# Kernel tuning notes

Measured on AMD Instinct MI355X. Metric: run time of the kernel, lower is better.

## Reference

```python
import jax, jax.numpy as jnp
import numpy as np

B, T, D_MODEL = 2, 2048, 1024
H, D = 16, 64
NEG = -1e9


def setup_inputs() -> dict:
    key = jax.random.key(0)
    k1, k2, k3 = jax.random.split(key, 3)
    x = jax.random.normal(k1, (B, T, D_MODEL), dtype=jnp.float32)
    # causal additive bias: 0 at valid (j<=i), large negative otherwise
    causal = jnp.tril(jnp.ones((T, T), dtype=bool))
    mask = jnp.where(causal, 0.0, NEG).astype(jnp.float32)[None, None]
    # params (torch Linear no-bias; stored as [in, out] so y = x @ W)
    W_qkv = jax.random.normal(k2, (D_MODEL, H * 5 * D), dtype=jnp.float32) / np.sqrt(D_MODEL)
    W_out = jax.random.normal(k3, (H * D, D_MODEL), dtype=jnp.float32) / np.sqrt(H * D)
    lam = jnp.full((H,), 0.8, dtype=jnp.float32)
    return {"x": x, "mask": mask, "W_qkv": W_qkv, "W_out": W_out, "lam": lam}


def reference(x, mask, W_qkv, W_out, lam):
    scale = np.sqrt(D).astype(np.float32)
    qkv = (x @ W_qkv).reshape(B, T, H, 5 * D)          # (B,T,H,5D)
    q1, q2, k1, k2, v = (qkv[..., i * D:(i + 1) * D] for i in range(5))
    # scores: (B,H,T,T)
    s1 = jnp.einsum('bihd,bjhd->bhij', q1, k1) / scale + mask
    s2 = jnp.einsum('bihd,bjhd->bhij', q2, k2) / scale + mask
    a1 = jax.nn.softmax(s1, axis=-1)
    a2 = jax.nn.softmax(s2, axis=-1)
    lam_c = jnp.clip(lam, 0.0, 1.0)[None, :, None, None]
    attn = a1 - lam_c * a2
    out = jnp.einsum('bhij,bjhd->bihd', attn, v).reshape(B, T, H * D)
    return out @ W_out
```

## Files before the change

### kernel.cpp

```cpp
#include <hip/hip_runtime.h>


typedef __attribute__((ext_vector_type(8))) short short8;
typedef __attribute__((ext_vector_type(4))) float floatx4;
typedef __attribute__((ext_vector_type(2))) unsigned uintx2;

#define MFMA16(A_, B_, C_) __builtin_amdgcn_mfma_f32_16x16x32_bf16((A_), (B_), (C_), 0, 0, 0)

__device__ __forceinline__ unsigned short f2bf(float f) {
  unsigned u;
  __builtin_memcpy(&u, &f, 4);
  u += 0x7fffu + ((u >> 16) & 1u);
  return (unsigned short)(u >> 16);
}

__device__ __forceinline__ unsigned packbf2(float a, float b) {
  unsigned ua, ub;
  __builtin_memcpy(&ua, &a, 4);
  __builtin_memcpy(&ub, &b, 4);
  ua += 0x8000u;
  ub += 0x8000u;
  return __builtin_amdgcn_perm(ub, ua, 0x07060302u);
}

__device__ __forceinline__ void gload16(const unsigned short* g, void* l) {
  __builtin_amdgcn_global_load_lds(
      (const __attribute__((address_space(1))) void*)g,
      (__attribute__((address_space(3))) void*)l, 16, 0, 0);
}

__global__ __launch_bounds__(256) void cast_f32_bf16(const float* __restrict__ in,
                                                     unsigned short* __restrict__ out) {
  size_t i = ((size_t)blockIdx.x * 256 + threadIdx.x) * 8;
  float4 a0 = *(const float4*)(in + i);
  float4 a1 = *(const float4*)(in + i + 4);
  short8 v = {(short)f2bf(a0.x), (short)f2bf(a0.y), (short)f2bf(a0.z), (short)f2bf(a0.w),
              (short)f2bf(a1.x), (short)f2bf(a1.y), (short)f2bf(a1.z), (short)f2bf(a1.w)};
  *(short8*)(out + i) = v;
}

__global__ __launch_bounds__(256) void transpose_both(const float* __restrict__ wqkv,
                                                      unsigned short* __restrict__ wqkvT,
                                                      const float* __restrict__ wout,
                                                      unsigned short* __restrict__ woutT) {
  __shared__ unsigned short t[32][33];
  int bid = blockIdx.x;
  const float* in;
  unsigned short* out;
  int R = 1024, C;
  int bx, by;
  if (bid < 5120) {
    in = wqkv; out = wqkvT; C = 5120;
    bx = bid % 160; by = bid / 160;
  } else {
    bid -= 5120;
    in = wout; out = woutT; C = 1024;
    bx = bid % 32; by = bid / 32;
  }
  int c0 = bx * 32, r0 = by * 32;
  int tx = threadIdx.x & 31, ty = threadIdx.x >> 5;
#pragma unroll
  for (int i = 0; i < 4; i++) {
    int r = ty + i * 8;
    t[r][tx] = f2bf(in[(size_t)(r0 + r) * C + c0 + tx]);
  }
  __syncthreads();
#pragma unroll
  for (int i = 0; i < 4; i++) {
    int r = ty + i * 8;
    out[(size_t)(c0 + r) * R + r0 + tx] = t[tx][r];
  }
}

__global__ __launch_bounds__(256) void gemm_qkv(const unsigned short* __restrict__ A,
                                                const unsigned short* __restrict__ Bt,
                                                unsigned short* __restrict__ qkbuf,
                                                unsigned short* __restrict__ vtbuf) {
  const int tid = threadIdx.x;
  const int wave = tid >> 6, lane = tid & 63, lane15 = lane & 15, quad = lane >> 4;
  const int wr = wave >> 1, wc = wave & 1;
  const int bn = blockIdx.x % 40, bm = blockIdx.x / 40;
  const int row0 = bm * 128, col0 = bn * 128;
  __shared__ __align__(16) short S[2 * 128 * 64];
  short* As = S;
  short* Bs = S + 128 * 64;
  floatx4 acc[4][4] = {};
  const int srow = lane >> 3, scol = (lane & 7) * 8;
  const unsigned short* ga = A + (size_t)(row0 + wave * 32 + srow) * 1024 + scol;
  const unsigned short* gb = Bt + (size_t)(col0 + wave * 32 + srow) * 1024 + scol;
  short* lA = &As[wave * 32 * 64];
  short* lB = &Bs[wave * 32 * 64];
  for (int kt = 0; kt < 1024; kt += 64) {
    __syncthreads();
#pragma unroll
    for (int u = 0; u < 4; u++) {
      gload16(ga + (size_t)u * 8 * 1024 + kt, lA + u * 8 * 64);
      gload16(gb + (size_t)u * 8 * 1024 + kt, lB + u * 8 * 64);
    }
    __syncthreads();
#pragma unroll
    for (int kh = 0; kh < 2; kh++) {
      short8 af[4], bf[4];
#pragma unroll
      for (int mt = 0; mt < 4; mt++)
        af[mt] = *(const short8*)&As[(wr * 64 + mt * 16 + lane15) * 64 + kh * 32 + quad * 8];
#pragma unroll
      for (int nt = 0; nt < 4; nt++)
        bf[nt] = *(const short8*)&Bs[(wc * 64 + nt * 16 + lane15) * 64 + kh * 32 + quad * 8];
#pragma unroll
      for (int mt = 0; mt < 4; mt++)
#pragma unroll
        for (int nt = 0; nt < 4; nt++) acc[mt][nt] = MFMA16(af[mt], bf[nt], acc[mt][nt]);
    }
  }
  const int bn5 = bn % 5;
  const bool hasV = (bn5 == 2) || (bn5 == 4);
  const bool myV = hasV && (wc == ((bn5 == 4) ? 1 : 0));
  short* Svt = S;
  __syncthreads();
#pragma unroll
  for (int mt = 0; mt < 4; mt++)
#pragma unroll
    for (int nt = 0; nt < 4; nt++)
#pragma unroll
      for (int r = 0; r < 4; r++) {
        const int row = row0 + wr * 64 + mt * 16 + quad * 4 + r;
        const unsigned short v = f2bf(acc[mt][nt][r]);
        if (myV) {
          Svt[(nt * 16 + lane15) * 136 + wr * 64 + mt * 16 + quad * 4 + r] = (short)v;
        } else {
          const int col = col0 + wc * 64 + nt * 16 + lane15;
          const int h = col / 320, c = col % 320;
          qkbuf[(size_t)row * 4096 + h * 256 + c] = v;
        }
      }
  if (hasV) {
    __syncthreads();
    const int hV = 2 * (bn / 5) + (bn5 == 4);
    const int bb = row0 >> 11, t0 = row0 & 2047;
    const int d = tid >> 2, seg = tid & 3;
    unsigned short* gdst = vtbuf + (size_t)((bb * 16 + hV) * 64 + d) * 2048 + t0 + seg * 32;
#pragma unroll
    for (int k2 = 0; k2 < 4; k2++)
      *(short8*)(gdst + k2 * 8) = *(const short8*)&Svt[d * 136 + seg * 32 + k2 * 8];
  }
}

__global__ __launch_bounds__(256, 2) void attn_kernel(const unsigned short* __restrict__ qk,
                                                      const unsigned short* __restrict__ vt,
                                                      const float* __restrict__ lam,
                                                      unsigned short* __restrict__ attnout) {
  const int tid = threadIdx.x;
  const int wave = tid >> 6, lane = tid & 63, lane15 = lane & 15, quad = lane >> 4;
  const int bid = blockIdx.x;
  const int pr = bid >> 5, bh = bid & 31;
  const int h = bh & 15, b = bh >> 4;

  __shared__ __align__(16) short K12s[2][64 * 128];
  __shared__ __align__(16) short Vts[2][64 * 64];
  __shared__ __align__(16) short Ps[4][16 * 72];

  const float lamv = fminf(fmaxf(lam[h], 0.0f), 1.0f);

  const unsigned short* kbase = qk + (size_t)(b * 2048) * 4096 + h * 256 + 128;
  const unsigned short* vbase = vt + (size_t)((b * 16 + h) * 64) * 2048;

  const int klr = lane >> 4, kcp = (lane & 15) * 16;
  const int vlr = lane >> 3, vcp = (lane & 7) * 16;
  const int swz = (lane15 & 7) << 4;

  for (int sg = 0; sg < 2; sg++) {
    const int qt = sg ? (31 - pr) : pr;
    const int njt = qt + 1;
    const int qsub = qt * 4 + wave;

    const int qrow0 = qt * 64 + wave * 16;
    const unsigned short* qb = qk + (size_t)(b * 2048 + qrow0 + lane15) * 4096 + h * 256;
    const short8 q1f0 = *(const short8*)(qb + quad * 8);
    const short8 q1f1 = *(const short8*)(qb + 32 + quad * 8);
    const short8 q2f0 = *(const short8*)(qb + 64 + quad * 8);
    const short8 q2f1 = *(const short8*)(qb + 96 + quad * 8);

    floatx4 o1[4] = {}, o2[4] = {};
    float lp1 = 0.f, lp2 = 0.f;

    if (sg) __syncthreads();

#pragma unroll
    for (int u = 0; u < 4; u++) {
      const int c = u * 4 + wave, row = 4 * c + klr;
      gload16(kbase + (size_t)row * 4096 + ((kcp ^ ((row & 7) << 4)) >> 1), &K12s[0][c * 512]);
    }
#pragma unroll
    for (int u = 0; u < 2; u++) {
      const int c = u * 4 + wave, row = 8 * c + vlr;
      gload16(vbase + (size_t)row * 2048 + ((vcp ^ ((row & 7) << 4)) >> 1), &Vts[0][c * 512]);
    }

    int cur = 0;
    for (int jt = 0; jt < njt; jt++) {
      __syncthreads();
      if (jt + 1 < njt) {
        const int nb = cur ^ 1;
#pragma unroll
        for (int u = 0; u < 4; u++) {
          const int c = u * 4 + wave, row = 4 * c + klr;
          gload16(kbase + (size_t)((jt + 1) * 64 + row) * 4096 + ((kcp ^ ((row & 7) << 4)) >> 1),
                  &K12s[nb][c * 512]);
        }
#pragma unroll
        for (int u = 0; u < 2; u++) {
          const int c = u * 4 + wave, row = 8 * c + vlr;
          gload16(vbase + (size_t)row * 2048 + (jt + 1) * 64 + ((vcp ^ ((row & 7) << 4)) >> 1),
                  &Vts[nb][c * 512]);
        }
      }

      const int rel = qsub - 4 * jt;

      short8 vf[4][2];
#pragma unroll
      for (int nt = 0; nt < 4; nt++) {
        const short* vr = &Vts[cur][(nt * 16 + lane15) * 64];
        vf[nt][0] = *(const short8*)(vr + (((quad * 16) ^ swz) >> 1));
        vf[nt][1] = *(const short8*)(vr + (((64 + quad * 16) ^ swz) >> 1));
      }

      short* P = &Ps[wave][0];

#pragma unroll
      for (int mat = 0; mat < 2; mat++) {
        const int koffB = mat ? 128 : 0;
        const short8 qf0 = mat ? q2f0 : q1f0;
        const short8 qf1 = mat ? q2f1 : q1f1;
        float* lp = mat ? &lp2 : &lp1;
        floatx4* oo = mat ? o2 : o1;

#pragma unroll
        for (int ms = 0; ms < 4; ms++) {
          unsigned w0 = 0, w1 = 0;
          if (ms <= rel) {
            const short* kr = &K12s[cur][(ms * 16 + lane15) * 128];
            short8 k0 = *(const short8*)(kr + (((koffB + quad * 16) ^ swz) >> 1));
            short8 k1 = *(const short8*)(kr + (((koffB + 64 + quad * 16) ^ swz) >> 1));
            floatx4 s = {0.f, 0.f, 0.f, 0.f};
            s = MFMA16(k0, qf0, s);
            s = MFMA16(k1, qf1, s);
            float e[4];
#pragma unroll
            for (int r = 0; r < 4; r++)
              e[r] = __builtin_amdgcn_exp2f(s[r] * 0.18033688011112042f);
            if (ms == rel) {
              const int jq = quad * 4;
#pragma unroll
              for (int r = 0; r < 4; r++) e[r] = (jq + r <= lane15) ? e[r] : 0.0f;
            }
            *lp += (e[0] + e[1]) + (e[2] + e[3]);
            w0 = packbf2(e[0], e[1]);
            w1 = packbf2(e[2], e[3]);
          }
          uintx2 wv = {w0, w1};
          *(uintx2*)&P[lane15 * 72 + ms * 16 + quad * 4] = wv;
        }
        const short8 pa0 = *(const short8*)&P[lane15 * 72 + quad * 8];
        const short8 pa1 = *(const short8*)&P[lane15 * 72 + 32 + quad * 8];
#pragma unroll
        for (int nt = 0; nt < 4; nt++) oo[nt] = MFMA16(pa0, vf[nt][0], oo[nt]);
        if (rel >= 2) {
#pragma unroll
          for (int nt = 0; nt < 4; nt++) oo[nt] = MFMA16(pa1, vf[nt][1], oo[nt]);
        }
      }
      cur ^= 1;
    }

    lp1 += __shfl_xor(lp1, 16, 64);
    lp1 += __shfl_xor(lp1, 32, 64);
    lp2 += __shfl_xor(lp2, 16, 64);
    lp2 += __shfl_xor(lp2, 32, 64);

#pragma unroll
    for (int r = 0; r < 4; r++) {
      const float l1 = __shfl(lp1, quad * 4 + r, 64);
      const float l2 = __shfl(lp2, quad * 4 + r, 64);
      const float rl1 = __builtin_amdgcn_rcpf(l1);
      const float rl2 = lamv * __builtin_amdgcn_rcpf(l2);
      const int row = b * 2048 + qrow0 + quad * 4 + r;
#pragma unroll
      for (int nt = 0; nt < 4; nt++) {
        float v = o1[nt][r] * rl1 - o2[nt][r] * rl2;
        attnout[(size_t)row * 1024 + h * 64 + nt * 16 + lane15] = f2bf(v);
      }
    }
  }
}

__global__ __launch_bounds__(256) void gemm_out(const unsigned short* __restrict__ A,
                                                const unsigned short* __restrict__ Bt,
                                                float* __restrict__ Cout) {
  const int tid = threadIdx.x;
  const int wave = tid >> 6, lane = tid & 63, lane15 = lane & 15, quad = lane >> 4;
  const int wr = wave >> 1, wc = wave & 1;
  const int bn = blockIdx.x & 7, bm = blockIdx.x >> 3;
  const int row0 = bm * 64, col0 = bn * 128;
  __shared__ __align__(16) short As[64 * 64];
  __shared__ __align__(16) short Bs[128 * 64];
  floatx4 acc[2][4] = {};
  const int slr = lane >> 3, scl = (lane & 7) * 8;
  for (int kt = 0; kt < 1024; kt += 64) {
    __syncthreads();
#pragma unroll
    for (int u = 0; u < 2; u++) {
      const int c = wave * 2 + u;
      gload16(A + (size_t)(row0 + 8 * c + slr) * 1024 + kt + scl, &As[c * 512]);
    }
#pragma unroll
    for (int u = 0; u < 4; u++) {
      const int c = wave * 4 + u;
      gload16(Bt + (size_t)(col0 + 8 * c + slr) * 1024 + kt + scl, &Bs[c * 512]);
    }
    __syncthreads();
#pragma unroll
    for (int kh = 0; kh < 2; kh++) {
      short8 af[2], bf[4];
#pragma unroll
      for (int mt = 0; mt < 2; mt++)
        af[mt] = *(const short8*)&As[(wr * 32 + mt * 16 + lane15) * 64 + kh * 32 + quad * 8];
#pragma unroll
      for (int nt = 0; nt < 4; nt++)
        bf[nt] = *(const short8*)&Bs[(wc * 64 + nt * 16 + lane15) * 64 + kh * 32 + quad * 8];
#pragma unroll
      for (int mt = 0; mt < 2; mt++)
#pragma unroll
        for (int nt = 0; nt < 4; nt++) acc[mt][nt] = MFMA16(af[mt], bf[nt], acc[mt][nt]);
    }
  }
#pragma unroll
  for (int mt = 0; mt < 2; mt++)
#pragma unroll
    for (int nt = 0; nt < 4; nt++)
#pragma unroll
      for (int r = 0; r < 4; r++) {
        int row = row0 + wr * 32 + mt * 16 + quad * 4 + r;
        int col = col0 + wc * 64 + nt * 16 + lane15;
        Cout[(size_t)row * 1024 + col] = acc[mt][nt][r];
      }
}

extern "C" void kernel_launch(void* const* d_in, const int* in_sizes, int n_in,
                              void* d_out, int out_size, void* d_ws, size_t ws_size,
                              hipStream_t stream) {
  const float* x = (const float*)d_in[0];
  const float* Wqkv = (const float*)d_in[2];
  const float* Wout = (const float*)d_in[3];
  const float* lam = (const float*)d_in[4];
  float* out = (float*)d_out;

  unsigned short* ws = (unsigned short*)d_ws;
  unsigned short* WqkvT = ws;
  unsigned short* WoutT = WqkvT + (size_t)5120 * 1024;
  unsigned short* qkbuf = WoutT + (size_t)1024 * 1024;
  unsigned short* vtbuf = qkbuf + (size_t)4096 * 4096;
  unsigned short* xb = vtbuf + (size_t)2 * 16 * 64 * 2048;
  unsigned short* attnbuf = xb;

  cast_f32_bf16<<<2048, 256, 0, stream>>>(x, xb);
  transpose_both<<<5120 + 1024, 256, 0, stream>>>(Wqkv, WqkvT, Wout, WoutT);
  gemm_qkv<<<32 * 40, 256, 0, stream>>>(xb, WqkvT, qkbuf, vtbuf);
  attn_kernel<<<512, 256, 0, stream>>>(qkbuf, vtbuf, lam, attnbuf);
  gemm_out<<<64 * 8, 256, 0, stream>>>(attnbuf, WoutT, out);
}
```

Before: 263.3 us.

## Retile QKV GEMM to 256x256 blocks with double-buffered swizzled LDS

The QKV projection GEMM moves from 128x128 tiles with 4 waves to 256x256 tiles with 8 waves. It double-buffers the global-to-LDS loads using explicit vmcnt waits, XOR-swizzles the LDS layout to avoid bank conflicts, and raises MFMA issue priority. The V-transpose epilogue is remapped to the new per-wave head/column grouping. This targets load latency and LDS conflicts in the GEMM. The cost is 128KB of LDS and fewer blocks (320) on the GPU, which may underfill the CUs.

Result: faster. 251.6 us (-4.4%).

```diff
diff --git a/kernel.cpp b/kernel.cpp
--- a/kernel.cpp
+++ b/kernel.cpp
@@ -72,77 +72,106 @@
   }
 }
 
-__global__ __launch_bounds__(256) void gemm_qkv(const unsigned short* __restrict__ A,
-                                                const unsigned short* __restrict__ Bt,
-                                                unsigned short* __restrict__ qkbuf,
-                                                unsigned short* __restrict__ vtbuf) {
+__global__ __launch_bounds__(512, 2) void gemm_qkv(const unsigned short* __restrict__ A,
+                                                   const unsigned short* __restrict__ Bt,
+                                                   unsigned short* __restrict__ qkbuf,
+                                                   unsigned short* __restrict__ vtbuf) {
   const int tid = threadIdx.x;
   const int wave = tid >> 6, lane = tid & 63, lane15 = lane & 15, quad = lane >> 4;
-  const int wr = wave >> 1, wc = wave & 1;
-  const int bn = blockIdx.x % 40, bm = blockIdx.x / 40;
-  const int row0 = bm * 128, col0 = bn * 128;
-  __shared__ __align__(16) short S[2 * 128 * 64];
-  short* As = S;
-  short* Bs = S + 128 * 64;
-  floatx4 acc[4][4] = {};
-  const int srow = lane >> 3, scol = (lane & 7) * 8;
-  const unsigned short* ga = A + (size_t)(row0 + wave * 32 + srow) * 1024 + scol;
-  const unsigned short* gb = Bt + (size_t)(col0 + wave * 32 + srow) * 1024 + scol;
-  short* lA = &As[wave * 32 * 64];
-  short* lB = &Bs[wave * 32 * 64];
-  for (int kt = 0; kt < 1024; kt += 64) {
-    __syncthreads();
+  const int wm = wave >> 2, wn = wave & 3;
+  const int bn = blockIdx.x % 20, bm = blockIdx.x / 20;
+  const int row0 = bm * 256, col0 = bn * 256;
+  __shared__ __align__(16) short SMEM[65536];
+  floatx4 acc[8][4] = {};
+
+  const int srow = lane >> 3;
+  const int sseg = ((lane & 7) ^ srow) * 8;
+  const unsigned short* gA = A + (size_t)(row0 + srow) * 1024 + sseg;
+  const unsigned short* gB = Bt + (size_t)(col0 + srow) * 1024 + sseg;
+
+  auto stage = [&](int bufidx, int kt) {
 #pragma unroll
     for (int u = 0; u < 4; u++) {
-      gload16(ga + (size_t)u * 8 * 1024 + kt, lA + u * 8 * 64);
-      gload16(gb + (size_t)u * 8 * 1024 + kt, lB + u * 8 * 64);
-    }
-    __syncthreads();
+      const int c = wave * 4 + u;
+      gload16(gA + (size_t)c * 8192 + kt, &SMEM[bufidx * 16384 + c * 512]);
+      gload16(gB + (size_t)c * 8192 + kt, &SMEM[32768 + bufidx * 16384 + c * 512]);
+    }
+  };
+
+  stage(0, 0);
+  stage(1, 64);
+
+  const int swz = (lane15 & 7) << 3;
+  for (int t = 0; t < 16; t++) {
+    if (t < 15) {
+      asm volatile("s_waitcnt vmcnt(8)" ::: "memory");
+    } else {
+      asm volatile("s_waitcnt vmcnt(0)" ::: "memory");
+    }
+    __builtin_amdgcn_s_barrier();
+    const short* Ab = &SMEM[(t & 1) * 16384];
+    const short* Bb = &SMEM[32768 + (t & 1) * 16384];
 #pragma unroll
     for (int kh = 0; kh < 2; kh++) {
-      short8 af[4], bf[4];
-#pragma unroll
-      for (int mt = 0; mt < 4; mt++)
-        af[mt] = *(const short8*)&As[(wr * 64 + mt * 16 + lane15) * 64 + kh * 32 + quad * 8];
+      short8 bf[4];
 #pragma unroll
       for (int nt = 0; nt < 4; nt++)
-        bf[nt] = *(const short8*)&Bs[(wc * 64 + nt * 16 + lane15) * 64 + kh * 32 + quad * 8];
-#pragma unroll
-      for (int mt = 0; mt < 4; mt++)
-#pragma unroll
-        for (int nt = 0; nt < 4; nt++) acc[mt][nt] = MFMA16(af[mt], bf[nt], acc[mt][nt]);
-    }
-  }
-  const int bn5 = bn % 5;
-  const bool hasV = (bn5 == 2) || (bn5 == 4);
-  const bool myV = hasV && (wc == ((bn5 == 4) ? 1 : 0));
-  short* Svt = S;
+        bf[nt] =
+            *(const short8*)&Bb[(wn * 64 + nt * 16 + lane15) * 64 + ((kh * 32 + quad * 8) ^ swz)];
+#pragma unroll
+      for (int mh = 0; mh < 2; mh++) {
+        short8 af[4];
+#pragma unroll
+        for (int mt = 0; mt < 4; mt++)
+          af[mt] = *(const short8*)&Ab[(wm * 128 + mh * 64 + mt * 16 + lane15) * 64 +
+                                       ((kh * 32 + quad * 8) ^ swz)];
+        __builtin_amdgcn_s_setprio(1);
+#pragma unroll
+        for (int mt = 0; mt < 4; mt++)
+#pragma unroll
+          for (int nt = 0; nt < 4; nt++)
+            acc[mh * 4 + mt][nt] = MFMA16(af[mt], bf[nt], acc[mh * 4 + mt][nt]);
+        __builtin_amdgcn_s_setprio(0);
+      }
+    }
+    __builtin_amdgcn_s_barrier();
+    if (t + 2 < 16) stage(t & 1, (t + 2) * 64);
+  }
+
+  const int G = bn * 4 + wn;
+  const int g5 = G % 5, h = G / 5;
+  short* Svt = SMEM;
+  if (g5 != 4) {
+#pragma unroll
+    for (int m = 0; m < 8; m++)
+#pragma unroll
+      for (int nt = 0; nt < 4; nt++)
+#pragma unroll
+        for (int r = 0; r < 4; r++) {
+          const int row = row0 + wm * 128 + m * 16 + quad * 4 + r;
+          const int cq = g5 * 64 + nt * 16 + lane15;
+          qkbuf[(size_t)row * 4096 + h * 256 + cq] = f2bf(acc[m][nt][r]);
+        }
+  } else {
+#pragma unroll
+    for (int m = 0; m < 8; m++)
+#pragma unroll
+      for (int nt = 0; nt < 4; nt++)
+#pragma unroll
+        for (int r = 0; r < 4; r++)
+          Svt[(nt * 16 + lane15) * 264 + wm * 128 + m * 16 + quad * 4 + r] =
+              (short)f2bf(acc[m][nt][r]);
+  }
   __syncthreads();
-#pragma unroll
-  for (int mt = 0; mt < 4; mt++)
-#pragma unroll
-    for (int nt = 0; nt < 4; nt++)
-#pragma unroll
-      for (int r = 0; r < 4; r++) {
-        const int row = row0 + wr * 64 + mt * 16 + quad * 4 + r;
-        const unsigned short v = f2bf(acc[mt][nt][r]);
-        if (myV) {
-          Svt[(nt * 16 + lane15) * 136 + wr * 64 + mt * 16 + quad * 4 + r] = (short)v;
-        } else {
-          const int col = col0 + wc * 64 + nt * 16 + lane15;
-          const int h = col / 320, c = col % 320;
-          qkbuf[(size_t)row * 4096 + h * 256 + c] = v;
-        }
-      }
-  if (hasV) {
-    __syncthreads();
-    const int hV = 2 * (bn / 5) + (bn5 == 4);
+  if ((bn % 5) != 0) {
+    const int wnV = (4 + bn) % 5;
+    const int hV = (4 * bn + wnV) / 5;
     const int bb = row0 >> 11, t0 = row0 & 2047;
-    const int d = tid >> 2, seg = tid & 3;
-    unsigned short* gdst = vtbuf + (size_t)((bb * 16 + hV) * 64 + d) * 2048 + t0 + seg * 32;
-#pragma unroll
-    for (int k2 = 0; k2 < 4; k2++)
-      *(short8*)(gdst + k2 * 8) = *(const short8*)&Svt[d * 136 + seg * 32 + k2 * 8];
+    const int d = tid >> 3, sg = (tid & 7) * 32;
+    unsigned short* gdst = vtbuf + (size_t)((bb * 16 + hV) * 64 + d) * 2048 + t0 + sg;
+#pragma unroll
+    for (int u2 = 0; u2 < 4; u2++)
+      *(short8*)(gdst + u2 * 8) = *(const short8*)&Svt[d * 264 + sg + u2 * 8];
   }
 }
 
@@ -366,7 +395,7 @@
 
   cast_f32_bf16<<<2048, 256, 0, stream>>>(x, xb);
   transpose_both<<<5120 + 1024, 256, 0, stream>>>(Wqkv, WqkvT, Wout, WoutT);
-  gemm_qkv<<<32 * 40, 256, 0, stream>>>(xb, WqkvT, qkbuf, vtbuf);
+  gemm_qkv<<<16 * 20, 512, 0, stream>>>(xb, WqkvT, qkbuf, vtbuf);
   attn_kernel<<<512, 256, 0, stream>>>(qkbuf, vtbuf, lam, attnbuf);
   gemm_out<<<64 * 8, 256, 0, stream>>>(attnbuf, WoutT, out);
 }
```
